# Performance work log

Hardware: AMD Instinct MI355X
Metric: run time of the kernel (lower is better)

Reference implementation:

```python
import jax, jax.numpy as jnp
import numpy as np

B, N, D, H = 8, 1024, 1024, 16
DH = D // H
REL_VOCAB = 6  # stadia + 2
NEG_INF = -1e9


def setup_inputs() -> dict:
    key = jax.random.key(0)
    ks = jax.random.split(key, 8)
    hid = jax.random.normal(ks[0], (B, N, D), dtype=jnp.float32)
    adj = jax.random.randint(ks[1], (B, N, N), 0, 2, dtype=jnp.int32)
    relative_pos = jax.random.randint(ks[2], (B, N, N), 0, REL_VOCAB, dtype=jnp.int32)
    s = 1.0 / np.sqrt(D)
    Wq = jax.random.normal(ks[3], (D, D), dtype=jnp.float32) * s
    Wk = jax.random.normal(ks[4], (D, D), dtype=jnp.float32) * s
    Wv = jax.random.normal(ks[5], (D, D), dtype=jnp.float32) * s
    rel_table = jax.random.normal(ks[6], (REL_VOCAB, 1), dtype=jnp.float32)
    ln_gamma = jnp.ones((D,), dtype=jnp.float32)
    ln_beta = jnp.zeros((D,), dtype=jnp.float32)
    return {"hid": hid, "adj": adj, "relative_pos": relative_pos,
            "Wq": Wq, "Wk": Wk, "Wv": Wv, "rel_table": rel_table,
            "ln_gamma": ln_gamma, "ln_beta": ln_beta}


def _layer_norm(x, gamma, beta, eps=1e-5):
    mu = jnp.mean(x, axis=-1, keepdims=True)
    var = jnp.var(x, axis=-1, keepdims=True)
    return (x - mu) * jax.lax.rsqrt(var + eps) * gamma + beta


def reference(hid, adj, relative_pos, Wq, Wk, Wv, rel_table, ln_gamma, ln_beta):
    # relative position bias: embedding dim 1, squeezed -> [B, N, N]
    rel_bias = rel_table[relative_pos][..., 0]
    # projections, split into heads: [B, N, H, DH]
    q = (hid @ Wq).reshape(B, N, H, DH)
    k = (hid @ Wk).reshape(B, N, H, DH)
    v = (hid @ Wv).reshape(B, N, H, DH)
    # scores [B, H, N, N], scaled by sqrt(key_dim) = sqrt(D)
    scores = jnp.einsum('bqhd,bkhd->bhqk', q, k) / jnp.sqrt(jnp.float32(D))
    scores = scores + rel_bias[:, None, :, :]
    mask = (adj != 0)[:, None, :, :]
    scores = jnp.where(mask, scores, NEG_INF)
    attn = jax.nn.softmax(scores, axis=-1)
    out = jnp.einsum('bhqk,bkhd->bqhd', attn, v).reshape(B, N, D)
    out = jax.nn.relu(out) + hid  # activation + residual
    return _layer_norm(out, ln_gamma, ln_beta)
```

## Files before the change

kernel.cpp:

```cpp
#include <hip/hip_runtime.h>
#include <math.h>

#define Bc 8
#define Nc 1024
#define Dc 1024
#define Hc 16
#define DHc 64
#define NEGINF -1e9f

typedef unsigned int  u32;
typedef unsigned short u16;
typedef unsigned long long u64;
typedef u16  u16x8 __attribute__((ext_vector_type(8)));
typedef u16  u16x4 __attribute__((ext_vector_type(4)));
typedef u32  u32x2 __attribute__((ext_vector_type(2)));
typedef __bf16 bf16x8 __attribute__((ext_vector_type(8)));
typedef float f32x4 __attribute__((ext_vector_type(4)));

__device__ __forceinline__ u16 f2bf(float f) {
    u32 u = __builtin_bit_cast(u32, f);
    u += 0x7fffu + ((u >> 16) & 1u);
    return (u16)(u >> 16);
}
__device__ __forceinline__ float bf2f(u16 b) {
    return __builtin_bit_cast(float, (u32)b << 16);
}
__device__ __forceinline__ u32 pack2bf(float lo, float hi) {
    return __builtin_amdgcn_perm(__builtin_bit_cast(u32, hi),
                                 __builtin_bit_cast(u32, lo), 0x07060302u);
}

__device__ __forceinline__ void glds16(const u16* g, const u16* l) {
    __builtin_amdgcn_global_load_lds(
        (const __attribute__((address_space(1))) void*)(u64)g,
        (__attribute__((address_space(3))) void*)(u32)(u64)l, 16, 0, 0);
}

__global__ __launch_bounds__(256) void prep_fused(
    const int* __restrict__ adj, const int* __restrict__ relpos,
    const float* __restrict__ rel_table, u16* __restrict__ bias,
    const float* __restrict__ hid, u16* __restrict__ hidb,
    const float* __restrict__ Wq, const float* __restrict__ Wk,
    const float* __restrict__ Wv, u16* __restrict__ WqT,
    u16* __restrict__ WkT, u16* __restrict__ WvT)
{
    const int blk = blockIdx.x;
    const int t = threadIdx.x;

    if (blk < 8192) {
        __shared__ float tbl[8];
        if (t < 6) tbl[t] = rel_table[t];
        __syncthreads();
        int i = blk * 256 + t;
        int pos4 = i << 2;
        int row  = pos4 >> 10;
        int p    = pos4 & 1023;
        int blkb = p & ~63;
        int m    = (p & 63) >> 2;
        size_t base = ((size_t)row << 10) + blkb + m;
        u16x4 o;
#pragma unroll
        for (int j = 0; j < 4; ++j) {
            int a  = adj[base + 16 * j];
            int rp = relpos[base + 16 * j];
            o[j] = a ? f2bf(tbl[rp]) : f2bf(NEGINF);
        }
        ((u16x4*)bias)[i] = o;
    } else if (blk < 12288) {
        int idx = (blk - 8192) * 256 + t;
        float4 a = ((const float4*)hid)[2 * idx];
        float4 b = ((const float4*)hid)[2 * idx + 1];
        u16x8 o;
        o[0] = f2bf(a.x); o[1] = f2bf(a.y); o[2] = f2bf(a.z); o[3] = f2bf(a.w);
        o[4] = f2bf(b.x); o[5] = f2bf(b.y); o[6] = f2bf(b.z); o[7] = f2bf(b.w);
        ((u16x8*)hidb)[idx] = o;
    } else {
        __shared__ float tile[32][33];
        const int wb = blk - 12288;
        const int x = wb & 31, y = (wb >> 5) & 31, z = wb >> 10;
        const float* W; u16* WT;
        if (z == 0)      { W = Wq; WT = WqT; }
        else if (z == 1) { W = Wk; WT = WkT; }
        else             { W = Wv; WT = WvT; }
        const int tx = t & 31, ty = t >> 5;
        const int n0 = x * 32, k0 = y * 32;
#pragma unroll
        for (int i = 0; i < 4; ++i) {
            int r = ty + i * 8;
            tile[r][tx] = W[(size_t)(k0 + r) * Dc + n0 + tx];
        }
        __syncthreads();
#pragma unroll
        for (int i = 0; i < 4; ++i) {
            int n = ty + i * 8;
            WT[(size_t)(n0 + n) * Dc + k0 + tx] = f2bf(tile[tx][n]);
        }
    }
}

__global__ __launch_bounds__(256) void qkv_mfma(
    const u16* __restrict__ hidb, const u16* __restrict__ WqT,
    const u16* __restrict__ WkT, const u16* __restrict__ WvT,
    u16* __restrict__ qo, u16* __restrict__ ko, u16* __restrict__ vo)
{
    __shared__ u16 As[128 * 64];
    __shared__ u16 Bs[128 * 64];

    const int bx = blockIdx.x, by = blockIdx.y;
    const int z = bx >> 3;
    const int c0 = (bx << 7) & 1023;
    const int row0 = by << 7;
    const u16* WT; u16* out;
    if (z == 0)      { WT = WqT; out = qo; }
    else if (z == 1) { WT = WkT; out = ko; }
    else             { WT = WvT; out = vo; }

    const int tid = threadIdx.x;
    const int wave = tid >> 6, lane = tid & 63;
    const int g = lane >> 4, li = lane & 15;
    const int wr = wave >> 1, wc = wave & 1;
    const int lr = lane >> 3, ls = lane & 7;
    const int sseg = ls ^ lr;

    const u16* pa = hidb + (size_t)(row0 + wave * 32 + lr) * Dc + sseg * 8;
    const u16* pb = WT   + (size_t)(c0   + wave * 32 + lr) * Dc + sseg * 8;
    u16* la = &As[(wave * 32) * 64];
    u16* lb = &Bs[(wave * 32) * 64];

    f32x4 acc[4][4] = {};

    const int swz = (li & 7);

    for (int kt = 0; kt < Dc; kt += 64) {
        __syncthreads();
#pragma unroll
        for (int i = 0; i < 4; ++i) {
            glds16(pa + kt + i * 8 * Dc, la + i * 8 * 64);
            glds16(pb + kt + i * 8 * Dc, lb + i * 8 * 64);
        }
        __syncthreads();
#pragma unroll
        for (int ks = 0; ks < 2; ++ks) {
            const int soff = ((ks * 4 + g) ^ swz) * 8;
            bf16x8 af[4], bf[4];
#pragma unroll
            for (int mi = 0; mi < 4; ++mi)
                af[mi] = *(const bf16x8*)&As[(wr * 64 + mi * 16 + li) * 64 + soff];
#pragma unroll
            for (int nj = 0; nj < 4; ++nj)
                bf[nj] = *(const bf16x8*)&Bs[(wc * 64 + nj * 16 + li) * 64 + soff];
#pragma unroll
            for (int mi = 0; mi < 4; ++mi)
#pragma unroll
                for (int nj = 0; nj < 4; ++nj)
                    acc[mi][nj] = __builtin_amdgcn_mfma_f32_16x16x32_bf16(
                        af[mi], bf[nj], acc[mi][nj], 0, 0, 0);
        }
    }

    const int b = row0 >> 10;

    if (z != 2) {
        const int h2 = (c0 + wc * 64) >> 6;
        const int nbase = (row0 & 1023) + wr * 64 + g * 4;
#pragma unroll
        for (int mi = 0; mi < 4; ++mi)
#pragma unroll
            for (int rr = 0; rr < 4; ++rr) {
                int n = nbase + mi * 16 + rr;
                u32x2 pk;
                pk.x = (u32)f2bf(acc[mi][0][rr]) | ((u32)f2bf(acc[mi][1][rr]) << 16);
                pk.y = (u32)f2bf(acc[mi][2][rr]) | ((u32)f2bf(acc[mi][3][rr]) << 16);
                *(u32x2*)(out + ((size_t)(b * Hc + h2) * Nc + n) * DHc + 4 * li) = pk;
            }
    } else {
        __syncthreads();
        u16* T = ((wave & 2) ? Bs : As) + (wave & 1) * 4096;
#pragma unroll
        for (int mi = 0; mi < 4; ++mi)
#pragma unroll
            for (int rr = 0; rr < 4; ++rr) {
                int r = mi * 16 + g * 4 + rr;
                int pp = ((r & 15) << 2) | (r >> 4);
#pragma unroll
                for (int nj = 0; nj < 4; ++nj) {
                    int c = nj * 16 + li;
                    T[c * 64 + ((((pp >> 3) ^ (c & 7)) << 3) | (pp & 7))]
                        = f2bf(acc[mi][nj][rr]);
                }
            }
        const int nseg = ls ^ lr;
#pragma unroll
        for (int i = 0; i < 8; ++i) {
            int cl = i * 8 + lr;
            u16x8 val = *(const u16x8*)&T[cl * 64 + ls * 8];
            int cz = c0 + wc * 64 + cl;
            int n = (row0 & 1023) + wr * 64 + nseg * 8;
            *(u16x8*)&out[(((size_t)(b * Hc + (cz >> 6)) * DHc + (cz & 63)) * Nc) + n] = val;
        }
    }
}

__global__ __launch_bounds__(256, 3) void attn_mfma(
    const u16* __restrict__ q, const u16* __restrict__ k,
    const u16* __restrict__ v, const u16* __restrict__ bias,
    float* __restrict__ attn_out)
{
    __shared__ u16 Ks[2][64 * 64];
    __shared__ u16 VTs[2][64 * 64];
    __shared__ u16 PQ[128 * 72];

    const int tid = threadIdx.x;
    const int w = tid >> 6, lane = tid & 63;
    const int g = lane >> 4, li = lane & 15;
    const int lr8 = lane >> 3, ls8 = lane & 7;
    const int lseg = ls8 ^ lr8;

    const int id = blockIdx.x;
    const int b  = id & 7;
    const int r_ = id >> 3;
    const int h  = r_ & 15;
    const int qt = r_ >> 4;
    const int q0 = qt << 7;

    const float scale = 0.03125f;
    const u16* kbase = k + (size_t)(b * Hc + h) * Nc * DHc;
    const u16* vbase = v + (size_t)(b * Hc + h) * DHc * Nc;
    const u16* brow  = bias + ((size_t)(b * Nc) + q0 + w * 32) * Nc + 4 * li;

    {
        const u16* kp = kbase + (size_t)(w * 16 + lr8) * DHc + lseg * 8;
        const u16* vp = vbase + (size_t)(w * 16 + lr8) * Nc + lseg * 8;
        glds16(kp,           &Ks[0][(w * 16) * 64]);
        glds16(kp + 8 * DHc, &Ks[0][(w * 16) * 64 + 8 * 64]);
        glds16(vp,           &VTs[0][(w * 16) * 64]);
        glds16(vp + 8 * Nc,  &VTs[0][(w * 16) * 64 + 8 * 64]);
    }

    {
        const int sr = tid >> 1;
        const int sh = (tid & 1) * 32;
        const u16* qp = q + ((size_t)((b * Hc + h) * Nc) + q0 + sr) * DHc + sh;
        u16x8 a0 = *(const u16x8*)qp;
        u16x8 a1 = *(const u16x8*)(qp + 8);
        u16x8 a2 = *(const u16x8*)(qp + 16);
        u16x8 a3 = *(const u16x8*)(qp + 24);
        u16* dst = &PQ[sr * 72 + sh];
        *(u16x8*)(dst)      = a0; *(u16x8*)(dst + 8)  = a1;
        *(u16x8*)(dst + 16) = a2; *(u16x8*)(dst + 24) = a3;
    }

    u16x4 brv[2][4];
#pragma unroll
    for (int mt = 0; mt < 2; ++mt)
#pragma unroll
        for (int r = 0; r < 4; ++r)
            brv[mt][r] = *(const u16x4*)&brow[(size_t)(mt * 16 + g * 4 + r) * Nc];

    bf16x8 qf[2][2];
#pragma unroll
    for (int mt = 0; mt < 2; ++mt)
#pragma unroll
        for (int ks = 0; ks < 2; ++ks)
            qf[mt][ks] = *(const bf16x8*)&PQ[(w * 32 + mt * 16 + li) * 72 + ks * 32 + g * 8];

    f32x4 o_[2][4] = {};
    float lsum[2][4] = {};

    for (int it = 0; it < 16; ++it) {
        const int cur = it & 1;
        __syncthreads();

        u16x4 brn[2][4];
        if (it < 15) {
            const int k1 = (it + 1) * 64;
            const u16* kp = kbase + (size_t)(k1 + w * 16 + lr8) * DHc + lseg * 8;
            const u16* vp = vbase + (size_t)(w * 16 + lr8) * Nc + k1 + lseg * 8;
            u16* kl = &Ks[cur ^ 1][(w * 16) * 64];
            u16* vl = &VTs[cur ^ 1][(w * 16) * 64];
            glds16(kp,           kl);
            glds16(kp + 8 * DHc, kl + 8 * 64);
            glds16(vp,           vl);
            glds16(vp + 8 * Nc,  vl + 8 * 64);
#pragma unroll
            for (int mt = 0; mt < 2; ++mt)
#pragma unroll
                for (int r = 0; r < 4; ++r)
                    brn[mt][r] = *(const u16x4*)&brow[(size_t)(mt * 16 + g * 4 + r) * Nc + k1];
        }

        f32x4 sacc[2][4] = {};
#pragma unroll
        for (int ks = 0; ks < 2; ++ks) {
            const int so = (((ks << 2) | g) ^ (li & 7)) << 3;
#pragma unroll
            for (int nt = 0; nt < 4; ++nt) {
                bf16x8 kf = *(const bf16x8*)&Ks[cur][(nt * 16 + li) * 64 + so];
                sacc[0][nt] = __builtin_amdgcn_mfma_f32_16x16x32_bf16(qf[0][ks], kf, sacc[0][nt], 0, 0, 0);
                sacc[1][nt] = __builtin_amdgcn_mfma_f32_16x16x32_bf16(qf[1][ks], kf, sacc[1][nt], 0, 0, 0);
            }
        }

#pragma unroll
        for (int mt = 0; mt < 2; ++mt)
#pragma unroll
            for (int r = 0; r < 4; ++r) {
                const int qrl = mt * 16 + g * 4 + r;
                float pv[4];
#pragma unroll
                for (int nt = 0; nt < 4; ++nt) {
                    float sv = sacc[mt][nt][r] * scale + bf2f(brv[mt][r][nt]);
                    pv[nt] = __expf(sv);
                    lsum[mt][r] += pv[nt];
                }
                u32* dst = (u32*)&PQ[(w * 32 + qrl) * 72 + li * 4];
                dst[0] = pack2bf(pv[0], pv[1]);
                dst[1] = pack2bf(pv[2], pv[3]);
            }

#pragma unroll
        for (int ks = 0; ks < 2; ++ks) {
            const int so = (((ks << 2) | g) ^ (li & 7)) << 3;
            bf16x8 pa0 = *(const bf16x8*)&PQ[(w * 32 + li) * 72 + ks * 32 + g * 8];
            bf16x8 pa1 = *(const bf16x8*)&PQ[(w * 32 + 16 + li) * 72 + ks * 32 + g * 8];
#pragma unroll
            for (int j = 0; j < 4; ++j) {
                bf16x8 vf = *(const bf16x8*)&VTs[cur][(j * 16 + li) * 64 + so];
                o_[0][j] = __builtin_amdgcn_mfma_f32_16x16x32_bf16(pa0, vf, o_[0][j], 0, 0, 0);
                o_[1][j] = __builtin_amdgcn_mfma_f32_16x16x32_bf16(pa1, vf, o_[1][j], 0, 0, 0);
            }
        }

        if (it < 15) {
#pragma unroll
            for (int mt = 0; mt < 2; ++mt)
#pragma unroll
                for (int r = 0; r < 4; ++r)
                    brv[mt][r] = brn[mt][r];
        }
    }

#pragma unroll
    for (int mt = 0; mt < 2; ++mt)
#pragma unroll
        for (int r = 0; r < 4; ++r) {
            float l = lsum[mt][r];
            l += __shfl_xor(l, 1);
            l += __shfl_xor(l, 2);
            l += __shfl_xor(l, 4);
            l += __shfl_xor(l, 8);
            float inv = 1.f / l;
            int qrow = q0 + w * 32 + mt * 16 + g * 4 + r;
            float* op = attn_out + ((size_t)b * Nc + qrow) * Dc + h * DHc;
#pragma unroll
            for (int j = 0; j < 4; ++j)
                op[j * 16 + li] = o_[mt][j][r] * inv;
        }
}

__global__ __launch_bounds__(256) void ln_kernel(
    const float* attn_out, const float* __restrict__ hid,
    const float* __restrict__ gamma, const float* __restrict__ beta,
    float* out)
{
    const int row = blockIdx.x;
    const int t = threadIdx.x;

    float4 av = *(const float4*)&attn_out[(size_t)row * Dc + t * 4];
    float4 hv = *(const float4*)&hid[(size_t)row * Dc + t * 4];
    float x0 = fmaxf(av.x, 0.f) + hv.x;
    float x1 = fmaxf(av.y, 0.f) + hv.y;
    float x2 = fmaxf(av.z, 0.f) + hv.z;
    float x3 = fmaxf(av.w, 0.f) + hv.w;

    float s1 = x0 + x1 + x2 + x3;
    float s2 = x0 * x0 + x1 * x1 + x2 * x2 + x3 * x3;
#pragma unroll
    for (int off = 1; off < 64; off <<= 1) {
        s1 += __shfl_xor(s1, off);
        s2 += __shfl_xor(s2, off);
    }
    __shared__ float w1[4], w2[4];
    int lane = t & 63, wid = t >> 6;
    if (lane == 0) { w1[wid] = s1; w2[wid] = s2; }
    __syncthreads();
    s1 = w1[0] + w1[1] + w1[2] + w1[3];
    s2 = w2[0] + w2[1] + w2[2] + w2[3];

    float mu  = s1 * (1.f / 1024.f);
    float var = s2 * (1.f / 1024.f) - mu * mu;
    float rstd = rsqrtf(var + 1e-5f);

    float4 g  = *(const float4*)&gamma[t * 4];
    float4 be = *(const float4*)&beta[t * 4];
    float4 r4;
    r4.x = (x0 - mu) * rstd * g.x + be.x;
    r4.y = (x1 - mu) * rstd * g.y + be.y;
    r4.z = (x2 - mu) * rstd * g.z + be.z;
    r4.w = (x3 - mu) * rstd * g.w + be.w;
    *(float4*)&out[(size_t)row * Dc + t * 4] = r4;
}

extern "C" void kernel_launch(void* const* d_in, const int* in_sizes, int n_in,
                              void* d_out, int out_size, void* d_ws, size_t ws_size,
                              hipStream_t stream) {
    const float* hid       = (const float*)d_in[0];
    const int*   adj       = (const int*)d_in[1];
    const int*   relpos    = (const int*)d_in[2];
    const float* Wq        = (const float*)d_in[3];
    const float* Wk        = (const float*)d_in[4];
    const float* Wv        = (const float*)d_in[5];
    const float* rel_table = (const float*)d_in[6];
    const float* gamma     = (const float*)d_in[7];
    const float* beta      = (const float*)d_in[8];
    float* out = (float*)d_out;

    const size_t per  = (size_t)Bc * Hc * Nc * DHc;
    const size_t wsz  = (size_t)Dc * Dc;
    u16* qb   = (u16*)d_ws;
    u16* kb   = qb + per;
    u16* vb   = kb + per;
    u16* bias = vb + per;
    u16* hidb = bias + (size_t)Bc * Nc * Nc;
    u16* wqT  = hidb + (size_t)Bc * Nc * Dc;
    u16* wkT  = wqT + wsz;
    u16* wvT  = wkT + wsz;

    prep_fused<<<15360, 256, 0, stream>>>(adj, relpos, rel_table, bias,
                                          hid, hidb, Wq, Wk, Wv, wqT, wkT, wvT);
    qkv_mfma<<<dim3(24, 64), 256, 0, stream>>>(hidb, wqT, wkT, wvT, qb, kb, vb);
    attn_mfma<<<1024, 256, 0, stream>>>(qb, kb, vb, bias, out);
    ln_kernel<<<Bc * Nc, 256, 0, stream>>>(out, hid, gamma, beta, out);
}
```

Measured before the change: 284.9 us.

## Split QKV GEMM into QK and V kernels, fold scale into Q, add setprio

```diff
diff --git a/kernel.cpp b/kernel.cpp
--- a/kernel.cpp
+++ b/kernel.cpp
@@ -98,22 +98,20 @@
     }
 }
 
-__global__ __launch_bounds__(256) void qkv_mfma(
+__global__ __launch_bounds__(256) void qkv_qk(
     const u16* __restrict__ hidb, const u16* __restrict__ WqT,
-    const u16* __restrict__ WkT, const u16* __restrict__ WvT,
-    u16* __restrict__ qo, u16* __restrict__ ko, u16* __restrict__ vo)
+    const u16* __restrict__ WkT, u16* __restrict__ qo, u16* __restrict__ ko)
 {
     __shared__ u16 As[128 * 64];
     __shared__ u16 Bs[128 * 64];
 
-    const int bx = blockIdx.x, by = blockIdx.y;
-    const int z = bx >> 3;
-    const int c0 = (bx << 7) & 1023;
-    const int row0 = by << 7;
-    const u16* WT; u16* out;
-    if (z == 0)      { WT = WqT; out = qo; }
-    else if (z == 1) { WT = WkT; out = ko; }
-    else             { WT = WvT; out = vo; }
+    const int yy = blockIdx.y;
+    const int z = yy >> 3;
+    const int c0 = (yy & 7) << 7;
+    const int row0 = blockIdx.x << 7;
+    const u16* WT = z ? WkT : WqT;
+    u16* out      = z ? ko  : qo;
+    const float qsc = z ? 1.0f : 0.03125f;
 
     const int tid = threadIdx.x;
     const int wave = tid >> 6, lane = tid & 63;
@@ -159,45 +157,96 @@
     }
 
     const int b = row0 >> 10;
-
-    if (z != 2) {
-        const int h2 = (c0 + wc * 64) >> 6;
-        const int nbase = (row0 & 1023) + wr * 64 + g * 4;
-#pragma unroll
-        for (int mi = 0; mi < 4; ++mi)
-#pragma unroll
-            for (int rr = 0; rr < 4; ++rr) {
-                int n = nbase + mi * 16 + rr;
-                u32x2 pk;
-                pk.x = (u32)f2bf(acc[mi][0][rr]) | ((u32)f2bf(acc[mi][1][rr]) << 16);
-                pk.y = (u32)f2bf(acc[mi][2][rr]) | ((u32)f2bf(acc[mi][3][rr]) << 16);
-                *(u32x2*)(out + ((size_t)(b * Hc + h2) * Nc + n) * DHc + 4 * li) = pk;
+    const int h2 = (c0 + wc * 64) >> 6;
+    const int nbase = (row0 & 1023) + wr * 64 + g * 4;
+#pragma unroll
+    for (int mi = 0; mi < 4; ++mi)
+#pragma unroll
+        for (int rr = 0; rr < 4; ++rr) {
+            int n = nbase + mi * 16 + rr;
+            u32x2 pk;
+            pk.x = (u32)f2bf(acc[mi][0][rr] * qsc) | ((u32)f2bf(acc[mi][1][rr] * qsc) << 16);
+            pk.y = (u32)f2bf(acc[mi][2][rr] * qsc) | ((u32)f2bf(acc[mi][3][rr] * qsc) << 16);
+            *(u32x2*)(out + ((size_t)(b * Hc + h2) * Nc + n) * DHc + 4 * li) = pk;
+        }
+}
+
+__global__ __launch_bounds__(256) void qkv_v(
+    const u16* __restrict__ hidb, const u16* __restrict__ WvT,
+    u16* __restrict__ vo)
+{
+    __shared__ u16 As[128 * 64];
+    __shared__ u16 Bs[128 * 64];
+
+    const int c0 = blockIdx.y << 7;
+    const int row0 = blockIdx.x << 7;
+
+    const int tid = threadIdx.x;
+    const int wave = tid >> 6, lane = tid & 63;
+    const int g = lane >> 4, li = lane & 15;
+    const int wr = wave >> 1, wc = wave & 1;
+    const int lr = lane >> 3, ls = lane & 7;
+    const int sseg = ls ^ lr;
+
+    const u16* pa = hidb + (size_t)(row0 + wave * 32 + lr) * Dc + sseg * 8;
+    const u16* pb = WvT  + (size_t)(c0   + wave * 32 + lr) * Dc + sseg * 8;
+    u16* la = &As[(wave * 32) * 64];
+    u16* lb = &Bs[(wave * 32) * 64];
+
+    f32x4 acc[4][4] = {};
+    const int swz = (li & 7);
+
+    for (int kt = 0; kt < Dc; kt += 64) {
+        __syncthreads();
+#pragma unroll
+        for (int i = 0; i < 4; ++i) {
+            glds16(pa + kt + i * 8 * Dc, la + i * 8 * 64);
+            glds16(pb + kt + i * 8 * Dc, lb + i * 8 * 64);
+        }
+        __syncthreads();
+#pragma unroll
+        for (int ks = 0; ks < 2; ++ks) {
+            const int soff = ((ks * 4 + g) ^ swz) * 8;
+            bf16x8 af[4], bf[4];
+#pragma unroll
+            for (int mi = 0; mi < 4; ++mi)
+                af[mi] = *(const bf16x8*)&As[(wr * 64 + mi * 16 + li) * 64 + soff];
+#pragma unroll
+            for (int nj = 0; nj < 4; ++nj)
+                bf[nj] = *(const bf16x8*)&Bs[(wc * 64 + nj * 16 + li) * 64 + soff];
+#pragma unroll
+            for (int mi = 0; mi < 4; ++mi)
+#pragma unroll
+                for (int nj = 0; nj < 4; ++nj)
+                    acc[mi][nj] = __builtin_amdgcn_mfma_f32_16x16x32_bf16(
+                        af[mi], bf[nj], acc[mi][nj], 0, 0, 0);
+        }
+    }
+
+    const int b = row0 >> 10;
+    __syncthreads();
+    u16* T = ((wave & 2) ? Bs : As) + (wave & 1) * 4096;
+#pragma unroll
+    for (int mi = 0; mi < 4; ++mi)
+#pragma unroll
+        for (int rr = 0; rr < 4; ++rr) {
+            int r = mi * 16 + g * 4 + rr;
+            int pp = ((r & 15) << 2) | (r >> 4);
+#pragma unroll
+            for (int nj = 0; nj < 4; ++nj) {
+                int c = nj * 16 + li;
+                T[c * 64 + ((((pp >> 3) ^ (c & 7)) << 3) | (pp & 7))]
+                    = f2bf(acc[mi][nj][rr]);
             }
-    } else {
-        __syncthreads();
-        u16* T = ((wave & 2) ? Bs : As) + (wave & 1) * 4096;
-#pragma unroll
-        for (int mi = 0; mi < 4; ++mi)
-#pragma unroll
-            for (int rr = 0; rr < 4; ++rr) {
-                int r = mi * 16 + g * 4 + rr;
-                int pp = ((r & 15) << 2) | (r >> 4);
-#pragma unroll
-                for (int nj = 0; nj < 4; ++nj) {
-                    int c = nj * 16 + li;
-                    T[c * 64 + ((((pp >> 3) ^ (c & 7)) << 3) | (pp & 7))]
-                        = f2bf(acc[mi][nj][rr]);
-                }
-            }
-        const int nseg = ls ^ lr;
-#pragma unroll
-        for (int i = 0; i < 8; ++i) {
-            int cl = i * 8 + lr;
-            u16x8 val = *(const u16x8*)&T[cl * 64 + ls * 8];
-            int cz = c0 + wc * 64 + cl;
-            int n = (row0 & 1023) + wr * 64 + nseg * 8;
-            *(u16x8*)&out[(((size_t)(b * Hc + (cz >> 6)) * DHc + (cz & 63)) * Nc) + n] = val;
-        }
+        }
+    const int nseg = ls ^ lr;
+#pragma unroll
+    for (int i = 0; i < 8; ++i) {
+        int cl = i * 8 + lr;
+        u16x8 val = *(const u16x8*)&T[cl * 64 + ls * 8];
+        int cz = c0 + wc * 64 + cl;
+        int n = (row0 & 1023) + wr * 64 + nseg * 8;
+        *(u16x8*)&vo[(((size_t)(b * Hc + (cz >> 6)) * DHc + (cz & 63)) * Nc) + n] = val;
     }
 }
 
@@ -223,7 +272,6 @@
     const int qt = r_ >> 4;
     const int q0 = qt << 7;
 
-    const float scale = 0.03125f;
     const u16* kbase = k + (size_t)(b * Hc + h) * Nc * DHc;
     const u16* vbase = v + (size_t)(b * Hc + h) * DHc * Nc;
     const u16* brow  = bias + ((size_t)(b * Nc) + q0 + w * 32) * Nc + 4 * li;
@@ -290,6 +338,7 @@
         }
 
         f32x4 sacc[2][4] = {};
+        __builtin_amdgcn_s_setprio(1);
 #pragma unroll
         for (int ks = 0; ks < 2; ++ks) {
             const int so = (((ks << 2) | g) ^ (li & 7)) << 3;
@@ -300,6 +349,7 @@
                 sacc[1][nt] = __builtin_amdgcn_mfma_f32_16x16x32_bf16(qf[1][ks], kf, sacc[1][nt], 0, 0, 0);
             }
         }
+        __builtin_amdgcn_s_setprio(0);
 
 #pragma unroll
         for (int mt = 0; mt < 2; ++mt)
@@ -309,7 +359,7 @@
                 float pv[4];
 #pragma unroll
                 for (int nt = 0; nt < 4; ++nt) {
-                    float sv = sacc[mt][nt][r] * scale + bf2f(brv[mt][r][nt]);
+                    float sv = sacc[mt][nt][r] + bf2f(brv[mt][r][nt]);
                     pv[nt] = __expf(sv);
                     lsum[mt][r] += pv[nt];
                 }
@@ -318,6 +368,7 @@
                 dst[1] = pack2bf(pv[2], pv[3]);
             }
 
+        __builtin_amdgcn_s_setprio(1);
 #pragma unroll
         for (int ks = 0; ks < 2; ++ks) {
             const int so = (((ks << 2) | g) ^ (li & 7)) << 3;
@@ -330,6 +381,7 @@
                 o_[1][j] = __builtin_amdgcn_mfma_f32_16x16x32_bf16(pa1, vf, o_[1][j], 0, 0, 0);
             }
         }
+        __builtin_amdgcn_s_setprio(0);
 
         if (it < 15) {
 #pragma unroll
@@ -428,7 +480,8 @@
 
     prep_fused<<<15360, 256, 0, stream>>>(adj, relpos, rel_table, bias,
                                           hid, hidb, Wq, Wk, Wv, wqT, wkT, wvT);
-    qkv_mfma<<<dim3(24, 64), 256, 0, stream>>>(hidb, wqT, wkT, wvT, qb, kb, vb);
+    qkv_qk<<<dim3(64, 16), 256, 0, stream>>>(hidb, wqT, wkT, qb, kb);
+    qkv_v<<<dim3(64, 8), 256, 0, stream>>>(hidb, wvT, vb);
     attn_mfma<<<1024, 256, 0, stream>>>(qb, kb, vb, bias, out);
     ln_kernel<<<Bc * Nc, 256, 0, stream>>>(out, hid, gamma, beta, out);
 }
```

After: 293.4 us. 3.0% more time.
